# Optimization experiments

Hardware: AMD Instinct MI355X
Metric: run time of the kernel (lower is better)

## Reference

```python
import jax, jax.numpy as jnp
import numpy as np
from jax import lax

DIM = 128
TOPW = 4
SCALE = DIM ** (-0.5)


def setup_inputs() -> dict:
    key = jax.random.key(0)
    kq, ki = jax.random.split(key)
    query = jax.random.normal(kq, (4, 4096, DIM), dtype=jnp.float32)
    image = jax.random.normal(ki, (4, 8192, DIM), dtype=jnp.float32)
    return {"query": query, "image": image}


def reference(query, image):
    # diff_routing=False: inputs are detached in torch; no effect on fwd values.
    # attn: (b, Nq, mn) = scaled QK^T
    attn = jnp.einsum('bqc,bmc->bqm', query, image) * SCALE
    _, topw_index = lax.top_k(attn, TOPW)  # (b, Nq, topw)
    return topw_index
```

## Files before the change

kernel.cpp:

```cpp
#include <hip/hip_runtime.h>
#include <float.h>
#include <stdint.h>


#define NBATCH 4
#define NQ 4096
#define NM 8192
#define KD 128

typedef unsigned short ushort_t;
typedef __attribute__((ext_vector_type(8))) short bf16x8;
typedef __attribute__((ext_vector_type(4))) float f32x4;

#define BETTER64(v, i, w, j) (((v) > (w)) || ((v) == (w) && (i) < (j)))

__device__ inline float fmed3(float a, float b, float c) {
#if __has_builtin(__builtin_amdgcn_fmed3f)
  return __builtin_amdgcn_fmed3f(a, b, c);
#else
  return fmaxf(fminf(a, b), fminf(fmaxf(a, b), c));
#endif
}

__device__ inline ushort_t f2bf(float f) {
  unsigned u = __float_as_uint(f);
  u += 0x7fffu + ((u >> 16) & 1u);
  return (ushort_t)(u >> 16);
}

__global__ __launch_bounds__(256) void wr_cvt(const float* __restrict__ qry,
                                              const float* __restrict__ img,
                                              ushort_t* __restrict__ qb,
                                              int4* __restrict__ ib) {
  const int blk = (int)blockIdx.x;
  const int tid = (int)threadIdx.x;
  if (blk < 2048) {
    const int t = blk * 256 + tid;
    const float4 v = ((const float4*)qry)[t];
    ushort4 o;
    o.x = f2bf(v.x); o.y = f2bf(v.y); o.z = f2bf(v.z); o.w = f2bf(v.w);
    ((ushort4*)qb)[t] = o;
  } else {
    const int tg = blk - 2048;
    const int b = tg >> 8;
    const int tile = tg & 255;
    __shared__ __align__(16) ushort_t T[32 * 128];
    {
      const int r = tid >> 3;
      const int seg = tid & 7;
      const float* src = img + ((size_t)(b * NM + tile * 32 + r)) * KD + seg * 16;
      ushort_t tmp[16];
#pragma unroll
      for (int i = 0; i < 4; ++i) {
        const float4 v = ((const float4*)src)[i];
        tmp[i * 4 + 0] = f2bf(v.x);
        tmp[i * 4 + 1] = f2bf(v.y);
        tmp[i * 4 + 2] = f2bf(v.z);
        tmp[i * 4 + 3] = f2bf(v.w);
      }
      const int c0 = (seg * 16 + r * 8) & 127;
      const int c1 = (seg * 16 + 8 + r * 8) & 127;
      *(int4*)&T[r * 128 + c0] = *(const int4*)&tmp[0];
      *(int4*)&T[r * 128 + c1] = *(const int4*)&tmp[8];
    }
    __syncthreads();
    int4* dstt = ib + ((size_t)b * 256 + tile) * 512;
#pragma unroll
    for (int h = 0; h < 2; ++h) {
      const int n = tid + h * 256;
      const int l = n & 63;
      const int ks = (n >> 6) & 3;
      const int htl = n >> 8;
      const int row = htl * 16 + (l & 15);
      const int col = ks * 32 + (l >> 4) * 8;
      dstt[n] = *(const int4*)&T[row * 128 + ((col + row * 8) & 127)];
    }
  }
}

__global__ __launch_bounds__(512, 1) void wr_mfma(const float* __restrict__ qry,
                                                  const float* __restrict__ img,
                                                  const ushort_t* __restrict__ qb,
                                                  const int4* __restrict__ ib,
                                                  int* __restrict__ out) {
  const int bid = (int)blockIdx.x;
  const int b = (bid & 7) >> 1;
  const int qt = ((bid >> 3) << 1) | (bid & 1);
  const int qbase = qt * 64;

  const int tid = (int)threadIdx.x;
  const int lane = tid & 63;
  const int w = tid >> 6;
  const int q15 = lane & 15;
  const int quad = lane >> 4;

  const ushort_t* Qb = qb + ((size_t)b * NQ + qbase) * KD;
  const int4* ibc = ib + (size_t)b * 131072;

  bf16x8 bfrag[4][4];
#pragma unroll
  for (int s = 0; s < 4; ++s)
#pragma unroll
    for (int ks = 0; ks < 4; ++ks)
      bfrag[s][ks] =
          *(const bf16x8*)(Qb + (size_t)(s * 16 + q15) * KD + ks * 32 + quad * 8);

  float tch[4][4];
#pragma unroll
  for (int s = 0; s < 4; ++s)
#pragma unroll
    for (int e = 0; e < 4; ++e) tch[s][e] = -FLT_MAX;

  bf16x8 B0[4], B1[4], B2[4];

  auto loadH = [&](bf16x8* R, int h) {
    const int4* p = ibc + (((w * 64 + h) << 8) + lane);
#pragma unroll
    for (int ks = 0; ks < 4; ++ks) R[ks] = *(const bf16x8*)(p + ks * 64);
  };

  int hl = 3;
  int vb = 2047 - 4 * quad;

  auto step = [&](bf16x8* R) {
    f32x4 a[4];
#pragma unroll
    for (int s = 0; s < 4; ++s) a[s] = {0.f, 0.f, 0.f, 0.f};
#pragma unroll
    for (int ks = 0; ks < 4; ++ks)
#pragma unroll
      for (int s = 0; s < 4; ++s)
        a[s] = __builtin_amdgcn_mfma_f32_16x16x32_bf16(R[ks], bfrag[s][ks], a[s],
                                                       0, 0, 0);
    if (hl < 64) loadH(R, hl);
    ++hl;
#pragma unroll
    for (int s = 0; s < 4; ++s) {
#pragma unroll
      for (int r = 0; r < 4; ++r) {
        const unsigned kr = (unsigned)(vb - r);
        const float k =
            __uint_as_float((__float_as_uint(a[s][r]) & 0xFFFFF800u) | kr);
        tch[s][3] = fmed3(k, tch[s][2], tch[s][3]);
        tch[s][2] = fmed3(k, tch[s][1], tch[s][2]);
        tch[s][1] = fmed3(k, tch[s][0], tch[s][1]);
        tch[s][0] = fmaxf(tch[s][0], k);
      }
    }
    vb -= 16;
  };

  loadH(B0, 0);
  loadH(B1, 1);
  loadH(B2, 2);
  for (int g = 0; g < 21; ++g) { step(B0); step(B1); step(B2); }
  step(B0);

#pragma unroll
  for (int s = 0; s < 4; ++s) {
    float k4[4];
#pragma unroll
    for (int e = 0; e < 4; ++e) k4[e] = __shfl_down(tch[s][e], 32, 64);
#pragma unroll
    for (int e = 0; e < 4; ++e) {
      const float k = k4[e];
      tch[s][3] = fmed3(k, tch[s][2], tch[s][3]);
      tch[s][2] = fmed3(k, tch[s][1], tch[s][2]);
      tch[s][1] = fmed3(k, tch[s][0], tch[s][1]);
      tch[s][0] = fmaxf(tch[s][0], k);
    }
#pragma unroll
    for (int e = 0; e < 4; ++e) k4[e] = __shfl_down(tch[s][e], 16, 64);
#pragma unroll
    for (int e = 0; e < 4; ++e) {
      const float k = k4[e];
      tch[s][3] = fmed3(k, tch[s][2], tch[s][3]);
      tch[s][2] = fmed3(k, tch[s][1], tch[s][2]);
      tch[s][1] = fmed3(k, tch[s][0], tch[s][1]);
      tch[s][0] = fmaxf(tch[s][0], k);
    }
  }

  __shared__ float ck[64][33];
  __shared__ int top8[64][8];
  __shared__ double pd[64][8];
  __shared__ int pi[64][8];

  if (lane < 16) {
#pragma unroll
    for (int s = 0; s < 4; ++s)
#pragma unroll
      for (int e = 0; e < 4; ++e) ck[s * 16 + q15][w * 4 + e] = tch[s][e];
  }
  __syncthreads();

  for (int p = tid; p < 2048; p += 512) {
    const int q = p >> 5;
    const int j = p & 31;
    const float k = ck[q][j];
    int rank = 0;
#pragma unroll 8
    for (int i = 0; i < 32; ++i) {
      const float o = ck[q][i];
      rank += (o > k) || (o == k && i < j);
    }
    if (rank < 8) {
      const unsigned bits = __float_as_uint(k);
      top8[q][rank] = (j >> 2) * 1024 + 2047 - (int)(bits & 0x7FFu);
    }
  }
  __syncthreads();

  {
    const int q = tid >> 3;
    const int slot = tid & 7;
    const int m = top8[q][slot];
    const float* qrow = qry + ((size_t)b * NQ + qbase + q) * KD;
    const float* irow = img + ((size_t)b * NM + m) * KD;
    double s0 = 0.0, s1 = 0.0, s2 = 0.0, s3 = 0.0;
#pragma unroll
    for (int k = 0; k < KD; k += 4) {
      const float4 xv = *(const float4*)(qrow + k);
      const float4 yv = *(const float4*)(irow + k);
      s0 = fma((double)xv.x, (double)yv.x, s0);
      s1 = fma((double)xv.y, (double)yv.y, s1);
      s2 = fma((double)xv.z, (double)yv.z, s2);
      s3 = fma((double)xv.w, (double)yv.w, s3);
    }
    pd[q][slot] = (s0 + s1) + (s2 + s3);
    pi[q][slot] = m;
  }
  __syncthreads();

  if (tid < 64) {
    const int q = tid;
    double fv[4];
    int fi[4];
#pragma unroll
    for (int e = 0; e < 4; ++e) { fv[e] = -DBL_MAX; fi[e] = 0x7fffffff; }
    for (int sl = 0; sl < 8; ++sl) {
      const double v = pd[q][sl];
      const int m = pi[q][sl];
      const bool b0 = BETTER64(v, m, fv[0], fi[0]);
      const bool b1 = BETTER64(v, m, fv[1], fi[1]);
      const bool b2 = BETTER64(v, m, fv[2], fi[2]);
      const bool b3 = BETTER64(v, m, fv[3], fi[3]);
      fv[3] = b2 ? fv[2] : (b3 ? v : fv[3]);
      fi[3] = b2 ? fi[2] : (b3 ? m : fi[3]);
      fv[2] = b1 ? fv[1] : (b2 ? v : fv[2]);
      fi[2] = b1 ? fi[1] : (b2 ? m : fi[2]);
      fv[1] = b0 ? fv[0] : (b1 ? v : fv[1]);
      fi[1] = b0 ? fi[0] : (b1 ? m : fi[1]);
      fv[0] = b0 ? v : fv[0];
      fi[0] = b0 ? m : fi[0];
    }
    int4 o;
    o.x = fi[0]; o.y = fi[1]; o.z = fi[2]; o.w = fi[3];
    *(int4*)(out + ((size_t)b * NQ + qbase + q) * 4) = o;
  }
}

#define QT 64
#define MT 128
#define KC 64
#define NTHREADS 512

__global__ __launch_bounds__(NTHREADS) void wr_main(const float* __restrict__ qry,
                                                    const float* __restrict__ img,
                                                    int* __restrict__ out) {
  __shared__ __align__(16) float A_lds[KD * QT];
  __shared__ __align__(16) float B_lds[KC * MT];

  const int t = (int)threadIdx.x;
  const int b = (int)blockIdx.x >> 6;
  const int qbase = ((int)blockIdx.x & 63) * QT;

  const float* qp = qry + ((size_t)b * NQ + qbase) * KD;
  const float* ip = img + (size_t)b * NM * KD;

  {
    const int r = t >> 3;
    const int kc = t & 7;
    const float* src = qp + (size_t)r * KD;
#pragma unroll
    for (int i = 0; i < 4; ++i) {
      const int k0 = kc * 4 + i * 32;
      const float4 v = *(const float4*)(src + k0);
      A_lds[(k0 + 0) * QT + r] = v.x;
      A_lds[(k0 + 1) * QT + r] = v.y;
      A_lds[(k0 + 2) * QT + r] = v.z;
      A_lds[(k0 + 3) * QT + r] = v.w;
    }
  }

  const int qi = t >> 5;
  const int mi = t & 31;

  float tv[4][4];
  int ti[4][4];
#pragma unroll
  for (int j = 0; j < 4; ++j)
#pragma unroll
    for (int s = 0; s < 4; ++s) { tv[j][s] = -FLT_MAX; ti[j][s] = 0x7fffffff; }

  for (int tile = 0; tile < NM / MT; ++tile) {
    const int mbase = tile * MT;
    float acc[4][4];
#pragma unroll
    for (int j = 0; j < 4; ++j)
#pragma unroll
      for (int s = 0; s < 4; ++s) acc[j][s] = 0.0f;

    for (int kb = 0; kb < KD; kb += KC) {
      __syncthreads();
      {
        const int r = t >> 2;
        const int kc = t & 3;
        const float* src = ip + (size_t)(mbase + r) * KD + kb;
#pragma unroll
        for (int i = 0; i < 4; ++i) {
          const int k0 = kc * 4 + i * 16;
          const float4 v = *(const float4*)(src + k0);
          B_lds[(k0 + 0) * MT + r] = v.x;
          B_lds[(k0 + 1) * MT + r] = v.y;
          B_lds[(k0 + 2) * MT + r] = v.z;
          B_lds[(k0 + 3) * MT + r] = v.w;
        }
      }
      __syncthreads();

#pragma unroll 8
      for (int k = 0; k < KC; ++k) {
        const float4 av = *(const float4*)&A_lds[(kb + k) * QT + qi * 4];
        const float4 bv = *(const float4*)&B_lds[k * MT + mi * 4];
        acc[0][0] = fmaf(av.x, bv.x, acc[0][0]);
        acc[0][1] = fmaf(av.x, bv.y, acc[0][1]);
        acc[0][2] = fmaf(av.x, bv.z, acc[0][2]);
        acc[0][3] = fmaf(av.x, bv.w, acc[0][3]);
        acc[1][0] = fmaf(av.y, bv.x, acc[1][0]);
        acc[1][1] = fmaf(av.y, bv.y, acc[1][1]);
        acc[1][2] = fmaf(av.y, bv.z, acc[1][2]);
        acc[1][3] = fmaf(av.y, bv.w, acc[1][3]);
        acc[2][0] = fmaf(av.z, bv.x, acc[2][0]);
        acc[2][1] = fmaf(av.z, bv.y, acc[2][1]);
        acc[2][2] = fmaf(av.z, bv.z, acc[2][2]);
        acc[2][3] = fmaf(av.z, bv.w, acc[2][3]);
        acc[3][0] = fmaf(av.w, bv.x, acc[3][0]);
        acc[3][1] = fmaf(av.w, bv.y, acc[3][1]);
        acc[3][2] = fmaf(av.w, bv.z, acc[3][2]);
        acc[3][3] = fmaf(av.w, bv.w, acc[3][3]);
      }
    }

#pragma unroll
    for (int j = 0; j < 4; ++j) {
#pragma unroll
      for (int s = 0; s < 4; ++s) {
        const float v = acc[j][s];
        const int m = mbase + mi * 4 + s;
        const bool b0 = v > tv[j][0];
        const bool b1 = v > tv[j][1];
        const bool b2 = v > tv[j][2];
        const bool b3 = v > tv[j][3];
        tv[j][3] = b2 ? tv[j][2] : (b3 ? v : tv[j][3]);
        ti[j][3] = b2 ? ti[j][2] : (b3 ? m : ti[j][3]);
        tv[j][2] = b1 ? tv[j][1] : (b2 ? v : tv[j][2]);
        ti[j][2] = b1 ? ti[j][1] : (b2 ? m : ti[j][2]);
        tv[j][1] = b0 ? tv[j][0] : (b1 ? v : tv[j][1]);
        ti[j][1] = b0 ? ti[j][0] : (b1 ? m : ti[j][1]);
        tv[j][0] = b0 ? v : tv[j][0];
        ti[j][0] = b0 ? m : ti[j][0];
      }
    }
  }

  __syncthreads();
  int* idx_lds = (int*)B_lds;
#pragma unroll
  for (int j = 0; j < 4; ++j)
#pragma unroll
    for (int s = 0; s < 4; ++s)
      idx_lds[(qi * 4 + j) * 128 + mi * 4 + s] = ti[j][s];
  __syncthreads();

  double* pv = (double*)A_lds;
  int* piL = (int*)(A_lds + 4096);
  {
    const int r = t >> 3;
    const int slot = t & 7;
    const float* qrow = qp + (size_t)r * KD;
    double bv[4];
    int bi[4];
#pragma unroll
    for (int e = 0; e < 4; ++e) { bv[e] = -DBL_MAX; bi[e] = 0x7fffffff; }

    for (int c = 0; c < 16; ++c) {
      const int m = idx_lds[r * 128 + slot * 16 + c];
      const float* irow = ip + (size_t)m * KD;
      double s0 = 0.0, s1 = 0.0, s2 = 0.0, s3 = 0.0;
#pragma unroll
      for (int k = 0; k < KD; k += 4) {
        const float4 xv = *(const float4*)(qrow + k);
        const float4 yv = *(const float4*)(irow + k);
        s0 = fma((double)xv.x, (double)yv.x, s0);
        s1 = fma((double)xv.y, (double)yv.y, s1);
        s2 = fma((double)xv.z, (double)yv.z, s2);
        s3 = fma((double)xv.w, (double)yv.w, s3);
      }
      const double v = (s0 + s1) + (s2 + s3);
      const bool b0 = BETTER64(v, m, bv[0], bi[0]);
      const bool b1 = BETTER64(v, m, bv[1], bi[1]);
      const bool b2 = BETTER64(v, m, bv[2], bi[2]);
      const bool b3 = BETTER64(v, m, bv[3], bi[3]);
      bv[3] = b2 ? bv[2] : (b3 ? v : bv[3]);
      bi[3] = b2 ? bi[2] : (b3 ? m : bi[3]);
      bv[2] = b1 ? bv[1] : (b2 ? v : bv[2]);
      bi[2] = b1 ? bi[1] : (b2 ? m : bi[2]);
      bv[1] = b0 ? bv[0] : (b1 ? v : bv[1]);
      bi[1] = b0 ? bi[0] : (b1 ? m : bi[1]);
      bv[0] = b0 ? v : bv[0];
      bi[0] = b0 ? m : bi[0];
    }
#pragma unroll
    for (int e = 0; e < 4; ++e) {
      pv[t * 4 + e] = bv[e];
      piL[t * 4 + e] = bi[e];
    }
  }
  __syncthreads();

  if (t < QT) {
    double fv[4];
    int fi[4];
#pragma unroll
    for (int e = 0; e < 4; ++e) { fv[e] = -DBL_MAX; fi[e] = 0x7fffffff; }
    for (int sl = 0; sl < 8; ++sl) {
#pragma unroll
      for (int e = 0; e < 4; ++e) {
        const double v = pv[(t * 8 + sl) * 4 + e];
        const int m = piL[(t * 8 + sl) * 4 + e];
        const bool b0 = BETTER64(v, m, fv[0], fi[0]);
        const bool b1 = BETTER64(v, m, fv[1], fi[1]);
        const bool b2 = BETTER64(v, m, fv[2], fi[2]);
        const bool b3 = BETTER64(v, m, fv[3], fi[3]);
        fv[3] = b2 ? fv[2] : (b3 ? v : fv[3]);
        fi[3] = b2 ? fi[2] : (b3 ? m : fi[3]);
        fv[2] = b1 ? fv[1] : (b2 ? v : fv[2]);
        fi[2] = b1 ? fi[1] : (b2 ? m : fi[2]);
        fv[1] = b0 ? fv[0] : (b1 ? v : fv[1]);
        fi[1] = b0 ? fi[0] : (b1 ? m : fi[1]);
        fv[0] = b0 ? v : fv[0];
        fi[0] = b0 ? m : fi[0];
      }
    }
    int4 o;
    o.x = fi[0]; o.y = fi[1]; o.z = fi[2]; o.w = fi[3];
    *(int4*)(out + ((size_t)b * NQ + qbase + t) * 4) = o;
  }
}

extern "C" void kernel_launch(void* const* d_in, const int* in_sizes, int n_in,
                              void* d_out, int out_size, void* d_ws, size_t ws_size,
                              hipStream_t stream) {
  const float* qry = (const float*)d_in[0];
  const float* img = (const float*)d_in[1];
  int* out = (int*)d_out;

  const size_t qbBytes = (size_t)NBATCH * NQ * KD * sizeof(ushort_t);
  const size_t ibBytes = (size_t)NBATCH * NM * KD * sizeof(ushort_t);

  if (ws_size >= qbBytes + ibBytes) {
    ushort_t* qb = (ushort_t*)d_ws;
    int4* ib = (int4*)((char*)d_ws + qbBytes);
    wr_cvt<<<3072, 256, 0, stream>>>(qry, img, qb, ib);
    wr_mfma<<<256, 512, 0, stream>>>(qry, img, qb, ib, out);
  } else {
    wr_main<<<NBATCH * (NQ / QT), NTHREADS, 0, stream>>>(qry, img, out);
  }
}
```

Before: 133.6 us.

## Select top-k over groups of four candidates and pipeline MFMA with selection

```diff
diff --git a/kernel.cpp b/kernel.cpp
--- a/kernel.cpp
+++ b/kernel.cpp
@@ -28,53 +28,42 @@
   return (ushort_t)(u >> 16);
 }
 
+__device__ inline unsigned pk2(float a, float b) {
+  return (unsigned)f2bf(a) | ((unsigned)f2bf(b) << 16);
+}
+
 __global__ __launch_bounds__(256) void wr_cvt(const float* __restrict__ qry,
                                               const float* __restrict__ img,
                                               ushort_t* __restrict__ qb,
                                               int4* __restrict__ ib) {
-  const int blk = (int)blockIdx.x;
-  const int tid = (int)threadIdx.x;
-  if (blk < 2048) {
-    const int t = blk * 256 + tid;
-    const float4 v = ((const float4*)qry)[t];
-    ushort4 o;
-    o.x = f2bf(v.x); o.y = f2bf(v.y); o.z = f2bf(v.z); o.w = f2bf(v.w);
-    ((ushort4*)qb)[t] = o;
+  const int t = (int)blockIdx.x * 256 + (int)threadIdx.x;
+  if (t < 524288) {
+    const int b = t >> 17;
+    const int tt = t & 131071;
+    const int tile = tt >> 9;
+    const int n = tt & 511;
+    const int l = n & 63;
+    const int m = tile * 32 + (n >> 8) * 16 + (l & 15);
+    const int k0 = ((n >> 6) & 3) * 32 + ((l >> 4) & 3) * 8;
+    const float* src = img + ((size_t)(b * NM + m)) * KD + k0;
+    const float4 v0 = *(const float4*)(src);
+    const float4 v1 = *(const float4*)(src + 4);
+    int4 o;
+    o.x = (int)pk2(v0.x, v0.y);
+    o.y = (int)pk2(v0.z, v0.w);
+    o.z = (int)pk2(v1.x, v1.y);
+    o.w = (int)pk2(v1.z, v1.w);
+    ib[t] = o;
   } else {
-    const int tg = blk - 2048;
-    const int b = tg >> 8;
-    const int tile = tg & 255;
-    __shared__ __align__(16) ushort_t T[32 * 128];
-    {
-      const int r = tid >> 3;
-      const int seg = tid & 7;
-      const float* src = img + ((size_t)(b * NM + tile * 32 + r)) * KD + seg * 16;
-      ushort_t tmp[16];
-#pragma unroll
-      for (int i = 0; i < 4; ++i) {
-        const float4 v = ((const float4*)src)[i];
-        tmp[i * 4 + 0] = f2bf(v.x);
-        tmp[i * 4 + 1] = f2bf(v.y);
-        tmp[i * 4 + 2] = f2bf(v.z);
-        tmp[i * 4 + 3] = f2bf(v.w);
-      }
-      const int c0 = (seg * 16 + r * 8) & 127;
-      const int c1 = (seg * 16 + 8 + r * 8) & 127;
-      *(int4*)&T[r * 128 + c0] = *(const int4*)&tmp[0];
-      *(int4*)&T[r * 128 + c1] = *(const int4*)&tmp[8];
-    }
-    __syncthreads();
-    int4* dstt = ib + ((size_t)b * 256 + tile) * 512;
-#pragma unroll
-    for (int h = 0; h < 2; ++h) {
-      const int n = tid + h * 256;
-      const int l = n & 63;
-      const int ks = (n >> 6) & 3;
-      const int htl = n >> 8;
-      const int row = htl * 16 + (l & 15);
-      const int col = ks * 32 + (l >> 4) * 8;
-      dstt[n] = *(const int4*)&T[row * 128 + ((col + row * 8) & 127)];
-    }
+    const int u = t - 524288;
+    const float4 v0 = ((const float4*)qry)[2 * u];
+    const float4 v1 = ((const float4*)qry)[2 * u + 1];
+    int4 o;
+    o.x = (int)pk2(v0.x, v0.y);
+    o.y = (int)pk2(v0.z, v0.w);
+    o.z = (int)pk2(v1.x, v1.y);
+    o.w = (int)pk2(v1.z, v1.w);
+    ((int4*)qb)[u] = o;
   }
 }
 
@@ -119,42 +108,66 @@
     for (int ks = 0; ks < 4; ++ks) R[ks] = *(const bf16x8*)(p + ks * 64);
   };
 
-  int hl = 3;
-  int vb = 2047 - 4 * quad;
-
-  auto step = [&](bf16x8* R) {
-    f32x4 a[4];
-#pragma unroll
-    for (int s = 0; s < 4; ++s) a[s] = {0.f, 0.f, 0.f, 0.f};
-#pragma unroll
-    for (int ks = 0; ks < 4; ++ks)
+  const f32x4 z4 = {0.f, 0.f, 0.f, 0.f};
+
+  auto mfma_all = [&](bf16x8* R, f32x4* acc) {
+#pragma unroll
+    for (int s = 0; s < 4; ++s)
+      acc[s] = __builtin_amdgcn_mfma_f32_16x16x32_bf16(R[0], bfrag[s][0], z4, 0, 0, 0);
+#pragma unroll
+    for (int ks = 1; ks < 4; ++ks)
 #pragma unroll
       for (int s = 0; s < 4; ++s)
-        a[s] = __builtin_amdgcn_mfma_f32_16x16x32_bf16(R[ks], bfrag[s][ks], a[s],
-                                                       0, 0, 0);
-    if (hl < 64) loadH(R, hl);
-    ++hl;
+        acc[s] = __builtin_amdgcn_mfma_f32_16x16x32_bf16(R[ks], bfrag[s][ks],
+                                                         acc[s], 0, 0, 0);
+  };
+
+  int gb = 2047 - quad;
+
+  auto select4 = [&](f32x4* sc) {
 #pragma unroll
     for (int s = 0; s < 4; ++s) {
-#pragma unroll
-      for (int r = 0; r < 4; ++r) {
-        const unsigned kr = (unsigned)(vb - r);
-        const float k =
-            __uint_as_float((__float_as_uint(a[s][r]) & 0xFFFFF800u) | kr);
-        tch[s][3] = fmed3(k, tch[s][2], tch[s][3]);
-        tch[s][2] = fmed3(k, tch[s][1], tch[s][2]);
-        tch[s][1] = fmed3(k, tch[s][0], tch[s][1]);
-        tch[s][0] = fmaxf(tch[s][0], k);
-      }
-    }
-    vb -= 16;
+      const float gm =
+          fmaxf(fmaxf(fmaxf(sc[s][0], sc[s][1]), sc[s][2]), sc[s][3]);
+      const float k =
+          __uint_as_float((__float_as_uint(gm) & 0xFFFFF800u) | (unsigned)gb);
+      tch[s][3] = fmed3(k, tch[s][2], tch[s][3]);
+      tch[s][2] = fmed3(k, tch[s][1], tch[s][2]);
+      tch[s][1] = fmed3(k, tch[s][0], tch[s][1]);
+      tch[s][0] = fmaxf(tch[s][0], k);
+    }
+    gb -= 4;
   };
+
+  f32x4 aA[4], aB[4];
+  int hl;
 
   loadH(B0, 0);
   loadH(B1, 1);
   loadH(B2, 2);
-  for (int g = 0; g < 21; ++g) { step(B0); step(B1); step(B2); }
-  step(B0);
+  mfma_all(B0, aA);
+  loadH(B0, 3);
+  hl = 4;
+
+  auto stepf = [&](bf16x8* R, f32x4* cur, f32x4* sel) {
+    mfma_all(R, cur);
+    if (hl < 64) loadH(R, hl);
+    ++hl;
+    select4(sel);
+  };
+
+  for (int g = 0; g < 10; ++g) {
+    stepf(B1, aB, aA);
+    stepf(B2, aA, aB);
+    stepf(B0, aB, aA);
+    stepf(B1, aA, aB);
+    stepf(B2, aB, aA);
+    stepf(B0, aA, aB);
+  }
+  stepf(B1, aB, aA);
+  stepf(B2, aA, aB);
+  stepf(B0, aB, aA);
+  select4(aB);
 
 #pragma unroll
   for (int s = 0; s < 4; ++s) {
@@ -183,8 +196,8 @@
 
   __shared__ float ck[64][33];
   __shared__ int top8[64][8];
-  __shared__ double pd[64][8];
-  __shared__ int pi[64][8];
+  __shared__ double pd[64][33];
+  __shared__ int pi[64][33];
 
   if (lane < 16) {
 #pragma unroll
@@ -206,7 +219,7 @@
     }
     if (rank < 8) {
       const unsigned bits = __float_as_uint(k);
-      top8[q][rank] = (j >> 2) * 1024 + 2047 - (int)(bits & 0x7FFu);
+      top8[q][rank] = (j >> 2) * 1024 + (2047 - (int)(bits & 0x7FFu)) * 4;
     }
   }
   __syncthreads();
@@ -214,21 +227,25 @@
   {
     const int q = tid >> 3;
     const int slot = tid & 7;
-    const int m = top8[q][slot];
+    const int mb = top8[q][slot];
     const float* qrow = qry + ((size_t)b * NQ + qbase + q) * KD;
-    const float* irow = img + ((size_t)b * NM + m) * KD;
-    double s0 = 0.0, s1 = 0.0, s2 = 0.0, s3 = 0.0;
-#pragma unroll
-    for (int k = 0; k < KD; k += 4) {
-      const float4 xv = *(const float4*)(qrow + k);
-      const float4 yv = *(const float4*)(irow + k);
-      s0 = fma((double)xv.x, (double)yv.x, s0);
-      s1 = fma((double)xv.y, (double)yv.y, s1);
-      s2 = fma((double)xv.z, (double)yv.z, s2);
-      s3 = fma((double)xv.w, (double)yv.w, s3);
-    }
-    pd[q][slot] = (s0 + s1) + (s2 + s3);
-    pi[q][slot] = m;
+#pragma unroll
+    for (int jj = 0; jj < 4; ++jj) {
+      const int m = mb + jj;
+      const float* irow = img + ((size_t)b * NM + m) * KD;
+      double s0 = 0.0, s1 = 0.0, s2 = 0.0, s3 = 0.0;
+#pragma unroll
+      for (int k = 0; k < KD; k += 4) {
+        const float4 xv = *(const float4*)(qrow + k);
+        const float4 yv = *(const float4*)(irow + k);
+        s0 = fma((double)xv.x, (double)yv.x, s0);
+        s1 = fma((double)xv.y, (double)yv.y, s1);
+        s2 = fma((double)xv.z, (double)yv.z, s2);
+        s3 = fma((double)xv.w, (double)yv.w, s3);
+      }
+      pd[q][slot * 4 + jj] = (s0 + s1) + (s2 + s3);
+      pi[q][slot * 4 + jj] = m;
+    }
   }
   __syncthreads();
 
@@ -238,7 +255,7 @@
     int fi[4];
 #pragma unroll
     for (int e = 0; e < 4; ++e) { fv[e] = -DBL_MAX; fi[e] = 0x7fffffff; }
-    for (int sl = 0; sl < 8; ++sl) {
+    for (int sl = 0; sl < 32; ++sl) {
       const double v = pd[q][sl];
       const int m = pi[q][sl];
       const bool b0 = BETTER64(v, m, fv[0], fi[0]);
```

Result: slower. 238.7 us (+78.6%).
